# Kernel tuning notes

Measured on AMD Instinct MI355X. Metric: run time of the kernel, lower is better.

## Reference

```python
import jax, jax.numpy as jnp
import numpy as np
import hashlib

MAX_HASH_VALUE = 2 ** 8  # 256
BATCH, MAX_LEN, EMB, HID, VOCAB = 32, 512, 256, 1024, 32000


def _hash_mod(flat_ids, algo):
    # SHA digest interpreted little-endian; only value mod 256 matters for the
    # downstream (h1 + k*h2) % 256, and mod 256 of a little-endian int is just
    # the first digest byte. We keep the full int.from_bytes for faithfulness.
    return np.array(
        [int.from_bytes(algo(str(int(v)).encode()).digest(), 'little') % MAX_HASH_VALUE
         for v in flat_ids],
        dtype=np.int64,
    )


def setup_inputs() -> dict:
    key = jax.random.key(0)
    k1, k2, k3 = jax.random.split(key, 3)
    input_ids = jax.random.randint(k1, (BATCH, MAX_LEN), 0, VOCAB, dtype=jnp.int64)
    W = jax.random.normal(k2, (HID, EMB), dtype=jnp.float32) * (1.0 / np.sqrt(EMB))
    b = jax.random.normal(k3, (HID,), dtype=jnp.float32) * 0.01
    return {"input_ids": input_ids, "W": W, "b": b}


def reference(input_ids, W, b):
    ids = np.asarray(input_ids)            # [B, L] int
    B, L = ids.shape
    flat = ids.reshape(-1)
    h1 = _hash_mod(flat, hashlib.sha256).reshape(B, L)   # [B, L] in [0,256)
    h2 = _hash_mod(flat, hashlib.sha224).reshape(B, L)
    k = jnp.arange(EMB, dtype=jnp.int64)                 # [E]
    # hash3[b,l,k] = (h1 + k*h2) % 256
    hash3 = ((jnp.asarray(h1)[:, :, None] + k[None, None, :] * jnp.asarray(h2)[:, :, None])
             % MAX_HASH_VALUE).astype(jnp.float32)        # [B, L, E]
    out = jnp.einsum('ble,he->blh', hash3, W) + b        # [B, L, H]
    return out
```

## Files before the change

kernel.cpp:

```cpp
#include <hip/hip_runtime.h>
#include <stdint.h>

typedef short bf16x8 __attribute__((ext_vector_type(8)));
typedef float f32x16 __attribute__((ext_vector_type(16)));

#define EMB 256
#define HID 1024

#define ROTR(x,n) (((x)>>(n))|((x)<<(32-(n))))
#define S0F(x) (ROTR((x),7)^ROTR((x),18)^((x)>>3))
#define S1F(x) (ROTR((x),17)^ROTR((x),19)^((x)>>10))

#define RND1(Kc, Wt) do {                                                          \
    uint32_t t1_ = sh + (ROTR(se,6)^ROTR(se,11)^ROTR(se,25))                       \
                   + ((se&sf)^(~se&sg)) + (Kc) + (Wt);                             \
    uint32_t t2_ = (ROTR(sa,2)^ROTR(sa,13)^ROTR(sa,22))                            \
                   + ((sa&sb)^(sa&sc)^(sb&sc));                                    \
    sh=sg; sg=sf; sf=se; se=sd+t1_; sd=sc; sc=sb; sb=sa; sa=t1_+t2_; } while (0)

#define WSXS(a,b,c,d) ((a) += S0F(b) + (c) + S1F(d))

__device__ __forceinline__ uint32_t rbf(float x) {
    uint32_t b = __float_as_uint(x);
    return (b + 0x7FFFu + ((b >> 16) & 1u)) >> 16;
}
__device__ __forceinline__ uint4 pack8(float4 a, float4 b) {
    uint4 q;
    q.x = rbf(a.x) | (rbf(a.y) << 16);
    q.y = rbf(a.z) | (rbf(a.w) << 16);
    q.z = rbf(b.x) | (rbf(b.y) << 16);
    q.w = rbf(b.z) | (rbf(b.w) << 16);
    return q;
}

#define MFMA(av,bv,acc) __builtin_amdgcn_mfma_f32_32x32x16_bf16(av,bv,acc,0,0,0)

__global__ __launch_bounds__(256, 1) void fused_kernel(const uint32_t* __restrict__ ids32,
                                                       const float* __restrict__ W,
                                                       const float* __restrict__ bias,
                                                       float* __restrict__ out) {
    __shared__ uint4 Albuf[4096];
    __shared__ uint4 Blbuf[4096];
    uint32_t* redf = (uint32_t*)(Blbuf + 2048);

    const int bid = blockIdx.x;
    const int bm = bid >> 1;
    const int nb0 = (bid & 1) * 512;
    const int tid = (int)threadIdx.x;
    const int wv = tid >> 6, lane = tid & 63, lrow = lane & 31, lh = lane >> 5;
    const int wm = (wv >> 1) * 64, wn = (wv & 1) * 64;
    const int lga = (wv >> 1) * 2, lgb = (wv & 1) * 2;
    const int rr = tid >> 1;
    const uint32_t st = tid & 1;
    const int ag = rr >> 5, aslot = rr & 31;

    float4 stgA[16], stgB[16];

#define ISSUE(dst, cc) do {                                                        \
    const float4* ws_ = reinterpret_cast<const float4*>(                           \
        W + (size_t)(nb0 + ((cc) >> 1) * 128 + rr) * EMB + ((cc) & 1) * 128 + (int)st * 64); \
    _Pragma("unroll") for (int i_ = 0; i_ < 16; ++i_) dst[i_] = ws_[i_]; } while (0)

#define WRITEB(src, cc) do {                                                       \
    uint4* bb_ = Blbuf + ((cc) & 1) * 2048 + (ag * 8) * 64 + aslot;                \
    _Pragma("unroll") for (int q_ = 0; q_ < 4; ++q_) {                             \
        uint4 h0_ = pack8(src[q_ * 4 + 0], src[q_ * 4 + 1]);                       \
        uint4 h1_ = pack8(src[q_ * 4 + 2], src[q_ * 4 + 3]);                       \
        bb_[((int)st * 4 + q_) * 64]      = h0_;                                   \
        bb_[((int)st * 4 + q_) * 64 + 32] = h1_; } } while (0)

#define MFMA_CHUNK(cc) do {                                                        \
    const uint4* bb_ = Blbuf + ((cc) & 1) * 2048;                                  \
    _Pragma("unroll") for (int ks_ = 0; ks_ < 8; ++ks_) {                          \
        bf16x8 av0 = *reinterpret_cast<const bf16x8*>(&Albuf[(lga * 16 + ((cc) & 1) * 8 + ks_) * 64 + lane]); \
        bf16x8 av1 = *reinterpret_cast<const bf16x8*>(&Albuf[((lga + 1) * 16 + ((cc) & 1) * 8 + ks_) * 64 + lane]); \
        bf16x8 bv0 = *reinterpret_cast<const bf16x8*>(&bb_[(lgb * 8 + ks_) * 64 + lane]); \
        bf16x8 bv1 = *reinterpret_cast<const bf16x8*>(&bb_[((lgb + 1) * 8 + ks_) * 64 + lane]); \
        acc00 = MFMA(av0, bv0, acc00); acc01 = MFMA(av0, bv1, acc01);              \
        acc10 = MFMA(av1, bv0, acc10); acc11 = MFMA(av1, bv1, acc11); } } while (0)

#define STORE_SUB(ss, bj0_, bj1_) do {                                             \
    const int n0s_ = nb0 + (ss) * 128 + wn;                                        \
    _Pragma("unroll") for (int r_ = 0; r_ < 16; ++r_) {                            \
        const int rowl_ = (r_ & 3) + 8 * (r_ >> 2) + 4 * lh;                       \
        const size_t o0_ = (size_t)(bm * 128 + wm + rowl_) * HID;                  \
        const size_t o1_ = o0_ + 32 * HID;                                         \
        out[o0_ + n0s_ + lrow]      = acc00[r_] + bj0_;                            \
        out[o0_ + n0s_ + 32 + lrow] = acc01[r_] + bj1_;                            \
        out[o1_ + n0s_ + lrow]      = acc10[r_] + bj0_;                            \
        out[o1_ + n0s_ + 32 + lrow] = acc11[r_] + bj1_; }                          \
    acc00 = (f32x16)(0.0f); acc01 = (f32x16)(0.0f);                                \
    acc10 = (f32x16)(0.0f); acc11 = (f32x16)(0.0f); } while (0)

    ISSUE(stgA, 0);

    {
        const uint4* ids4 = reinterpret_cast<const uint4*>(ids32);
        uint4 da = ids4[tid], db = ids4[tid + 256];
        uint32_t z = da.y | da.w | db.y | db.w;
        unsigned long long m = __ballot(z != 0u);
        if (lane == 0) redf[wv] = (m != 0ull) ? 1u : 0u;
    }
    __syncthreads();
    const bool is64 = (redf[0] | redf[1] | redf[2] | redf[3]) == 0u;

    const int tok = bm * 128 + rr;
    const uint32_t v = is64 ? ids32[2 * tok] : ids32[tok];

    const uint32_t q4 = __umulhi(v, 0xD1B71759u) >> 13;
    const uint32_t r4 = v - q4 * 10000u;
    const uint32_t q3 = __umulhi(r4, 0x10624DD3u) >> 6;
    const uint32_t r3 = r4 - q3 * 1000u;
    const uint32_t q2 = __umulhi(r3, 0x51EB851Fu) >> 5;
    const uint32_t r2 = r3 - q2 * 100u;
    const uint32_t q1 = __umulhi(r2, 0xCCCCCCCDu) >> 3;
    const uint32_t q0 = r2 - q1 * 10u;
    const uint32_t nd = v >= 10000u ? 5u : v >= 1000u ? 4u : v >= 100u ? 3u
                         : v >= 10u ? 2u : 1u;
    uint64_t M = ((uint64_t)(q4 + '0') << 56) | ((uint64_t)(q3 + '0') << 48) |
                 ((uint64_t)(q2 + '0') << 40) | ((uint64_t)(q1 + '0') << 32) |
                 ((uint64_t)(q0 + '0') << 24) | ((uint64_t)0x80u << 16);
    M <<= 8u * (5u - nd);

    uint32_t w0 = (uint32_t)(M >> 32), w1 = (uint32_t)M;
    uint32_t w2 = 0, w3 = 0, w4 = 0, w5 = 0, w6 = 0, w7 = 0;
    uint32_t w8 = 0, w9 = 0, w10 = 0, w11 = 0, w12 = 0, w13 = 0, w14 = 0;
    uint32_t w15 = nd * 8u;

    uint32_t sa = st ? 0xc1059ed8u : 0x6a09e667u;
    uint32_t sb = st ? 0x367cd507u : 0xbb67ae85u;
    uint32_t sc = st ? 0x3070dd17u : 0x3c6ef372u;
    uint32_t sd = st ? 0xf70e5939u : 0xa54ff53au;
    uint32_t se = st ? 0xffc00b31u : 0x510e527fu;
    uint32_t sf = st ? 0x68581511u : 0x9b05688cu;
    uint32_t sg = st ? 0x64f98fa7u : 0x1f83d9abu;
    uint32_t sh = st ? 0xbefa4fa4u : 0x5be0cd19u;

    RND1(0x428a2f98u, w0);  RND1(0x71374491u, w1);  RND1(0xb5c0fbcfu, w2);
    RND1(0xe9b5dba5u, w3);  RND1(0x3956c25bu, w4);  RND1(0x59f111f1u, w5);
    RND1(0x923f82a4u, w6);  RND1(0xab1c5ed5u, w7);  RND1(0xd807aa98u, w8);
    RND1(0x12835b01u, w9);  RND1(0x243185beu, w10); RND1(0x550c7dc3u, w11);
    RND1(0x72be5d74u, w12); RND1(0x80deb1feu, w13); RND1(0x9bdc06a7u, w14);
    RND1(0xc19bf174u, w15);
    WSXS(w0,w1,w9,w14);    RND1(0xe49b69c1u, w0);
    WSXS(w1,w2,w10,w15);   RND1(0xefbe4786u, w1);
    WSXS(w2,w3,w11,w0);    RND1(0x0fc19dc6u, w2);
    WSXS(w3,w4,w12,w1);    RND1(0x240ca1ccu, w3);
    WSXS(w4,w5,w13,w2);    RND1(0x2de92c6fu, w4);
    WSXS(w5,w6,w14,w3);    RND1(0x4a7484aau, w5);
    WSXS(w6,w7,w15,w4);    RND1(0x5cb0a9dcu, w6);
    WSXS(w7,w8,w0,w5);     RND1(0x76f988dau, w7);
    WSXS(w8,w9,w1,w6);     RND1(0x983e5152u, w8);
    WSXS(w9,w10,w2,w7);    RND1(0xa831c66du, w9);
    WSXS(w10,w11,w3,w8);   RND1(0xb00327c8u, w10);
    WSXS(w11,w12,w4,w9);   RND1(0xbf597fc7u, w11);
    WSXS(w12,w13,w5,w10);  RND1(0xc6e00bf3u, w12);
    WSXS(w13,w14,w6,w11);  RND1(0xd5a79147u, w13);
    WSXS(w14,w15,w7,w12);  RND1(0x06ca6351u, w14);
    WSXS(w15,w0,w8,w13);   RND1(0x14292967u, w15);
    WSXS(w0,w1,w9,w14);    RND1(0x27b70a85u, w0);
    WSXS(w1,w2,w10,w15);   RND1(0x2e1b2138u, w1);
    WSXS(w2,w3,w11,w0);    RND1(0x4d2c6dfcu, w2);
    WSXS(w3,w4,w12,w1);    RND1(0x53380d13u, w3);
    WSXS(w4,w5,w13,w2);    RND1(0x650a7354u, w4);
    WSXS(w5,w6,w14,w3);    RND1(0x766a0abbu, w5);
    WSXS(w6,w7,w15,w4);    RND1(0x81c2c92eu, w6);
    WSXS(w7,w8,w0,w5);     RND1(0x92722c85u, w7);
    WSXS(w8,w9,w1,w6);     RND1(0xa2bfe8a1u, w8);
    WSXS(w9,w10,w2,w7);    RND1(0xa81a664bu, w9);
    WSXS(w10,w11,w3,w8);   RND1(0xc24b8b70u, w10);
    WSXS(w11,w12,w4,w9);   RND1(0xc76c51a3u, w11);
    WSXS(w12,w13,w5,w10);  RND1(0xd192e819u, w12);
    WSXS(w13,w14,w6,w11);  RND1(0xd6990624u, w13);
    WSXS(w14,w15,w7,w12);  RND1(0xf40e3585u, w14);
    WSXS(w15,w0,w8,w13);   RND1(0x106aa070u, w15);
    WSXS(w0,w1,w9,w14);    RND1(0x19a4c116u, w0);
    WSXS(w1,w2,w10,w15);   RND1(0x1e376c08u, w1);
    WSXS(w2,w3,w11,w0);    RND1(0x2748774cu, w2);
    WSXS(w3,w4,w12,w1);    RND1(0x34b0bcb5u, w3);
    WSXS(w4,w5,w13,w2);    RND1(0x391c0cb3u, w4);
    WSXS(w5,w6,w14,w3);    RND1(0x4ed8aa4au, w5);
    WSXS(w6,w7,w15,w4);    RND1(0x5b9cca4fu, w6);
    WSXS(w7,w8,w0,w5);     RND1(0x682e6ff3u, w7);
    WSXS(w8,w9,w1,w6);     RND1(0x748f82eeu, w8);
    WSXS(w9,w10,w2,w7);    RND1(0x78a5636fu, w9);
    WSXS(w10,w11,w3,w8);   RND1(0x84c87814u, w10);
    WSXS(w11,w12,w4,w9);   RND1(0x8cc70208u, w11);
    WSXS(w12,w13,w5,w10);  RND1(0x90befffau, w12);
    WSXS(w13,w14,w6,w11);  RND1(0xa4506cebu, w13);
    WSXS(w14,w15,w7,w12);  RND1(0xbef9a3f7u, w14);
    WSXS(w15,w0,w8,w13);   RND1(0xc67178f2u, w15);

    const uint32_t hv = ((st ? 0xc1059ed8u : 0x6a09e667u) + sa) >> 24;
    const uint32_t hvo = __shfl_xor(hv, 1);
    const uint32_t hv1 = st ? hvo : hv;
    const uint32_t hv2 = st ? hv : hvo;

    {
        uint32_t val = (hv1 + (st ? ((hv2 << 7) & 255u) : 0u)) & 255u;
        const int kfb = (int)st * 8;
#define PAIR(dst) { uint32_t lo_ = val; uint32_t hi_ = (val + hv2) & 255u;        \
                    val = (hi_ + hv2) & 255u;                                     \
                    dst = (__float_as_uint((float)lo_) >> 16) |                   \
                          (__float_as_uint((float)hi_) & 0xFFFF0000u); }
#pragma unroll
        for (int q = 0; q < 8; ++q) {
            uint32_t c0_, c1_, c2_, c3_, c4_, c5_, c6_, c7_;
            PAIR(c0_); PAIR(c1_); PAIR(c2_); PAIR(c3_);
            PAIR(c4_); PAIR(c5_); PAIR(c6_); PAIR(c7_);
            uint4 qa; qa.x = c0_; qa.y = c1_; qa.z = c2_; qa.w = c3_;
            uint4 qb; qb.x = c4_; qb.y = c5_; qb.z = c6_; qb.w = c7_;
            Albuf[(ag * 16 + kfb + q) * 64 + aslot]      = qa;
            Albuf[(ag * 16 + kfb + q) * 64 + aslot + 32] = qb;
        }
#undef PAIR
    }

    WRITEB(stgA, 0);
    ISSUE(stgB, 1);

    const float b00 = bias[nb0 +   0 + wn + lrow], b01 = bias[nb0 +   0 + wn + 32 + lrow];
    const float b10 = bias[nb0 + 128 + wn + lrow], b11 = bias[nb0 + 128 + wn + 32 + lrow];
    const float b20 = bias[nb0 + 256 + wn + lrow], b21 = bias[nb0 + 256 + wn + 32 + lrow];
    const float b30 = bias[nb0 + 384 + wn + lrow], b31 = bias[nb0 + 384 + wn + 32 + lrow];

    f32x16 acc00 = (f32x16)(0.0f), acc01 = (f32x16)(0.0f);
    f32x16 acc10 = (f32x16)(0.0f), acc11 = (f32x16)(0.0f);

    __syncthreads();

    ISSUE(stgA, 2);  MFMA_CHUNK(0);                         WRITEB(stgB, 1); __syncthreads();
    ISSUE(stgB, 3);  MFMA_CHUNK(1); STORE_SUB(0, b00, b01); WRITEB(stgA, 2); __syncthreads();
    ISSUE(stgA, 4);  MFMA_CHUNK(2);                         WRITEB(stgB, 3); __syncthreads();
    ISSUE(stgB, 5);  MFMA_CHUNK(3); STORE_SUB(1, b10, b11); WRITEB(stgA, 4); __syncthreads();
    ISSUE(stgA, 6);  MFMA_CHUNK(4);                         WRITEB(stgB, 5); __syncthreads();
    ISSUE(stgB, 7);  MFMA_CHUNK(5); STORE_SUB(2, b20, b21); WRITEB(stgA, 6); __syncthreads();
                     MFMA_CHUNK(6);                         WRITEB(stgB, 7); __syncthreads();
                     MFMA_CHUNK(7); STORE_SUB(3, b30, b31);

#undef ISSUE
#undef WRITEB
#undef MFMA_CHUNK
#undef STORE_SUB
}

extern "C" void kernel_launch(void* const* d_in, const int* in_sizes, int n_in,
                              void* d_out, int out_size, void* d_ws, size_t ws_size,
                              hipStream_t stream) {
    const uint32_t* ids32 = (const uint32_t*)d_in[0];
    const float* W = (const float*)d_in[1];
    const float* bias = (const float*)d_in[2];
    float* out = (float*)d_out;
    (void)d_ws; (void)ws_size; (void)in_sizes; (void)n_in; (void)out_size;

    fused_kernel<<<256, 256, 0, stream>>>(ids32, W, bias, out);
}
```

Measured before the change: 36.40 us.

## Remap W staging to wave-contiguous LDS writes and use LDS-only barriers

Reassigns which thread loads which W elements so each wave writes a contiguous, lane-indexed LDS region with a single pack8 store per step, instead of the two-slot interleaved scatter. It also replaces __syncthreads with a barrier that waits only on LDS counters (lgkmcnt), so in-flight global W prefetches and output stores no longer have to drain at each barrier. The risk is correctness of the new mapping against the MFMA B-fragment layout, and the weaker barrier relies on global data being consumed only after later waits.

```diff
diff --git a/kernel.cpp b/kernel.cpp
--- a/kernel.cpp
+++ b/kernel.cpp
@@ -34,6 +34,11 @@
 }
 
 #define MFMA(av,bv,acc) __builtin_amdgcn_mfma_f32_32x32x16_bf16(av,bv,acc,0,0,0)
+
+#define BARRIER_LGKM() do {                                                        \
+    asm volatile("s_waitcnt lgkmcnt(0)" ::: "memory");                             \
+    __builtin_amdgcn_s_barrier();                                                  \
+    __builtin_amdgcn_sched_barrier(0); } while (0)
 
 __global__ __launch_bounds__(256, 1) void fused_kernel(const uint32_t* __restrict__ ids32,
                                                        const float* __restrict__ W,
@@ -57,17 +62,17 @@
     float4 stgA[16], stgB[16];
 
 #define ISSUE(dst, cc) do {                                                        \
-    const float4* ws_ = reinterpret_cast<const float4*>(                           \
-        W + (size_t)(nb0 + ((cc) >> 1) * 128 + rr) * EMB + ((cc) & 1) * 128 + (int)st * 64); \
-    _Pragma("unroll") for (int i_ = 0; i_ < 16; ++i_) dst[i_] = ws_[i_]; } while (0)
+    const float4* ws_ = reinterpret_cast<const float4*>(W)                         \
+        + ((size_t)(nb0 + ((cc) >> 1) * 128 + wv * 32 + lrow) * 64)                \
+        + ((cc) & 1) * 32 + lh * 2;                                                \
+    _Pragma("unroll") for (int q_ = 0; q_ < 8; ++q_) {                             \
+        dst[2 * q_]     = ws_[q_ * 4];                                             \
+        dst[2 * q_ + 1] = ws_[q_ * 4 + 1]; } } while (0)
 
 #define WRITEB(src, cc) do {                                                       \
-    uint4* bb_ = Blbuf + ((cc) & 1) * 2048 + (ag * 8) * 64 + aslot;                \
-    _Pragma("unroll") for (int q_ = 0; q_ < 4; ++q_) {                             \
-        uint4 h0_ = pack8(src[q_ * 4 + 0], src[q_ * 4 + 1]);                       \
-        uint4 h1_ = pack8(src[q_ * 4 + 2], src[q_ * 4 + 3]);                       \
-        bb_[((int)st * 4 + q_) * 64]      = h0_;                                   \
-        bb_[((int)st * 4 + q_) * 64 + 32] = h1_; } } while (0)
+    uint4* bb_ = Blbuf + ((cc) & 1) * 2048 + wv * 512 + lane;                      \
+    _Pragma("unroll") for (int q_ = 0; q_ < 8; ++q_)                               \
+        bb_[q_ * 64] = pack8(src[2 * q_], src[2 * q_ + 1]); } while (0)
 
 #define MFMA_CHUNK(cc) do {                                                        \
     const uint4* bb_ = Blbuf + ((cc) & 1) * 2048;                                  \
@@ -101,7 +106,7 @@
         unsigned long long m = __ballot(z != 0u);
         if (lane == 0) redf[wv] = (m != 0ull) ? 1u : 0u;
     }
-    __syncthreads();
+    BARRIER_LGKM();
     const bool is64 = (redf[0] | redf[1] | redf[2] | redf[3]) == 0u;
 
     const int tok = bm * 128 + rr;
@@ -227,15 +232,15 @@
     f32x16 acc00 = (f32x16)(0.0f), acc01 = (f32x16)(0.0f);
     f32x16 acc10 = (f32x16)(0.0f), acc11 = (f32x16)(0.0f);
 
-    __syncthreads();
-
-    ISSUE(stgA, 2);  MFMA_CHUNK(0);                         WRITEB(stgB, 1); __syncthreads();
-    ISSUE(stgB, 3);  MFMA_CHUNK(1); STORE_SUB(0, b00, b01); WRITEB(stgA, 2); __syncthreads();
-    ISSUE(stgA, 4);  MFMA_CHUNK(2);                         WRITEB(stgB, 3); __syncthreads();
-    ISSUE(stgB, 5);  MFMA_CHUNK(3); STORE_SUB(1, b10, b11); WRITEB(stgA, 4); __syncthreads();
-    ISSUE(stgA, 6);  MFMA_CHUNK(4);                         WRITEB(stgB, 5); __syncthreads();
-    ISSUE(stgB, 7);  MFMA_CHUNK(5); STORE_SUB(2, b20, b21); WRITEB(stgA, 6); __syncthreads();
-                     MFMA_CHUNK(6);                         WRITEB(stgB, 7); __syncthreads();
+    BARRIER_LGKM();
+
+    ISSUE(stgA, 2);  MFMA_CHUNK(0);                         WRITEB(stgB, 1); BARRIER_LGKM();
+    ISSUE(stgB, 3);  MFMA_CHUNK(1); STORE_SUB(0, b00, b01); WRITEB(stgA, 2); BARRIER_LGKM();
+    ISSUE(stgA, 4);  MFMA_CHUNK(2);                         WRITEB(stgB, 3); BARRIER_LGKM();
+    ISSUE(stgB, 5);  MFMA_CHUNK(3); STORE_SUB(1, b10, b11); WRITEB(stgA, 4); BARRIER_LGKM();
+    ISSUE(stgA, 6);  MFMA_CHUNK(4);                         WRITEB(stgB, 5); BARRIER_LGKM();
+    ISSUE(stgB, 7);  MFMA_CHUNK(5); STORE_SUB(2, b20, b21); WRITEB(stgA, 6); BARRIER_LGKM();
+                     MFMA_CHUNK(6);                         WRITEB(stgB, 7); BARRIER_LGKM();
                      MFMA_CHUNK(7); STORE_SUB(3, b30, b31);
 
 #undef ISSUE
```

Measured after the change: 39.36 us. 8.1% more time.

## Halve M tile to 64 rows and run two blocks per CU

Applied to the files above, without the earlier changes.

Shrinks each block's output tile from 128 to 64 rows, doubling the grid to 512 blocks. Each wave now computes a 32x64 sub-tile with two accumulators instead of four. Shared buffers are halved and launch bounds are raised to two blocks per CU, so more waves can hide memory latency. W is staged in 64-wide K chunks over 16 pipeline steps, and only half the threads run the SHA hashing. The cost is that every W tile is re-read by twice as many blocks, with more barriers per block.

```diff
diff --git a/kernel.cpp b/kernel.cpp
--- a/kernel.cpp
+++ b/kernel.cpp
@@ -35,62 +35,54 @@
 
 #define MFMA(av,bv,acc) __builtin_amdgcn_mfma_f32_32x32x16_bf16(av,bv,acc,0,0,0)
 
-__global__ __launch_bounds__(256, 1) void fused_kernel(const uint32_t* __restrict__ ids32,
+__global__ __launch_bounds__(256, 2) void fused_kernel(const uint32_t* __restrict__ ids32,
                                                        const float* __restrict__ W,
                                                        const float* __restrict__ bias,
                                                        float* __restrict__ out) {
-    __shared__ uint4 Albuf[4096];
-    __shared__ uint4 Blbuf[4096];
-    uint32_t* redf = (uint32_t*)(Blbuf + 2048);
+    __shared__ uint4 Albuf[2048];
+    __shared__ uint4 Blbuf[2048];
+    uint32_t* redf = (uint32_t*)(Blbuf + 1024);
 
     const int bid = blockIdx.x;
     const int bm = bid >> 1;
     const int nb0 = (bid & 1) * 512;
     const int tid = (int)threadIdx.x;
     const int wv = tid >> 6, lane = tid & 63, lrow = lane & 31, lh = lane >> 5;
-    const int wm = (wv >> 1) * 64, wn = (wv & 1) * 64;
-    const int lga = (wv >> 1) * 2, lgb = (wv & 1) * 2;
-    const int rr = tid >> 1;
-    const uint32_t st = tid & 1;
-    const int ag = rr >> 5, aslot = rr & 31;
-
-    float4 stgA[16], stgB[16];
+    const int lgb = (wv & 1) * 2;
+    const int mrow0 = bm * 64 + (wv >> 1) * 32;
+
+    float4 stgA[8], stgB[8];
 
 #define ISSUE(dst, cc) do {                                                        \
-    const float4* ws_ = reinterpret_cast<const float4*>(                           \
-        W + (size_t)(nb0 + ((cc) >> 1) * 128 + rr) * EMB + ((cc) & 1) * 128 + (int)st * 64); \
-    _Pragma("unroll") for (int i_ = 0; i_ < 16; ++i_) dst[i_] = ws_[i_]; } while (0)
+    const float4* ws_ = reinterpret_cast<const float4*>(W)                         \
+        + ((size_t)(nb0 + ((cc) >> 2) * 128 + wv * 32 + lrow) * 64)                \
+        + ((cc) & 3) * 16 + lh * 2;                                                \
+    _Pragma("unroll") for (int w_ = 0; w_ < 4; ++w_) {                             \
+        dst[2 * w_]     = ws_[w_ * 4];                                             \
+        dst[2 * w_ + 1] = ws_[w_ * 4 + 1]; } } while (0)
 
 #define WRITEB(src, cc) do {                                                       \
-    uint4* bb_ = Blbuf + ((cc) & 1) * 2048 + (ag * 8) * 64 + aslot;                \
-    _Pragma("unroll") for (int q_ = 0; q_ < 4; ++q_) {                             \
-        uint4 h0_ = pack8(src[q_ * 4 + 0], src[q_ * 4 + 1]);                       \
-        uint4 h1_ = pack8(src[q_ * 4 + 2], src[q_ * 4 + 3]);                       \
-        bb_[((int)st * 4 + q_) * 64]      = h0_;                                   \
-        bb_[((int)st * 4 + q_) * 64 + 32] = h1_; } } while (0)
+    uint4* bb_ = Blbuf + ((cc) & 1) * 1024 + wv * 256 + lane;                      \
+    _Pragma("unroll") for (int w_ = 0; w_ < 4; ++w_)                               \
+        bb_[w_ * 64] = pack8(src[2 * w_], src[2 * w_ + 1]); } while (0)
 
 #define MFMA_CHUNK(cc) do {                                                        \
-    const uint4* bb_ = Blbuf + ((cc) & 1) * 2048;                                  \
-    _Pragma("unroll") for (int ks_ = 0; ks_ < 8; ++ks_) {                          \
-        bf16x8 av0 = *reinterpret_cast<const bf16x8*>(&Albuf[(lga * 16 + ((cc) & 1) * 8 + ks_) * 64 + lane]); \
-        bf16x8 av1 = *reinterpret_cast<const bf16x8*>(&Albuf[((lga + 1) * 16 + ((cc) & 1) * 8 + ks_) * 64 + lane]); \
-        bf16x8 bv0 = *reinterpret_cast<const bf16x8*>(&bb_[(lgb * 8 + ks_) * 64 + lane]); \
-        bf16x8 bv1 = *reinterpret_cast<const bf16x8*>(&bb_[((lgb + 1) * 8 + ks_) * 64 + lane]); \
-        acc00 = MFMA(av0, bv0, acc00); acc01 = MFMA(av0, bv1, acc01);              \
-        acc10 = MFMA(av1, bv0, acc10); acc11 = MFMA(av1, bv1, acc11); } } while (0)
+    const uint4* bb_ = Blbuf + ((cc) & 1) * 1024;                                  \
+    const uint4* aa_ = Albuf + ((size_t)((wv >> 1) * 16 + ((cc) & 3) * 4)) * 64 + lane; \
+    _Pragma("unroll") for (int kf_ = 0; kf_ < 4; ++kf_) {                          \
+        bf16x8 av  = *reinterpret_cast<const bf16x8*>(&aa_[kf_ * 64]);             \
+        bf16x8 bv0 = *reinterpret_cast<const bf16x8*>(&bb_[(lgb * 4 + kf_) * 64 + lane]); \
+        bf16x8 bv1 = *reinterpret_cast<const bf16x8*>(&bb_[((lgb + 1) * 4 + kf_) * 64 + lane]); \
+        acc0 = MFMA(av, bv0, acc0); acc1 = MFMA(av, bv1, acc1); } } while (0)
 
 #define STORE_SUB(ss, bj0_, bj1_) do {                                             \
-    const int n0s_ = nb0 + (ss) * 128 + wn;                                        \
+    const int col_ = nb0 + (ss) * 128 + lgb * 32 + lrow;                           \
     _Pragma("unroll") for (int r_ = 0; r_ < 16; ++r_) {                            \
         const int rowl_ = (r_ & 3) + 8 * (r_ >> 2) + 4 * lh;                       \
-        const size_t o0_ = (size_t)(bm * 128 + wm + rowl_) * HID;                  \
-        const size_t o1_ = o0_ + 32 * HID;                                         \
-        out[o0_ + n0s_ + lrow]      = acc00[r_] + bj0_;                            \
-        out[o0_ + n0s_ + 32 + lrow] = acc01[r_] + bj1_;                            \
-        out[o1_ + n0s_ + lrow]      = acc10[r_] + bj0_;                            \
-        out[o1_ + n0s_ + 32 + lrow] = acc11[r_] + bj1_; }                          \
-    acc00 = (f32x16)(0.0f); acc01 = (f32x16)(0.0f);                                \
-    acc10 = (f32x16)(0.0f); acc11 = (f32x16)(0.0f); } while (0)
+        const size_t o_ = (size_t)(mrow0 + rowl_) * HID + col_;                    \
+        out[o_]      = acc0[r_] + bj0_;                                            \
+        out[o_ + 32] = acc1[r_] + bj1_; }                                          \
+    acc0 = (f32x16)(0.0f); acc1 = (f32x16)(0.0f); } while (0)
 
     ISSUE(stgA, 0);
 
@@ -104,99 +96,108 @@
     __syncthreads();
     const bool is64 = (redf[0] | redf[1] | redf[2] | redf[3]) == 0u;
 
-    const int tok = bm * 128 + rr;
-    const uint32_t v = is64 ? ids32[2 * tok] : ids32[tok];
-
-    const uint32_t q4 = __umulhi(v, 0xD1B71759u) >> 13;
-    const uint32_t r4 = v - q4 * 10000u;
-    const uint32_t q3 = __umulhi(r4, 0x10624DD3u) >> 6;
-    const uint32_t r3 = r4 - q3 * 1000u;
-    const uint32_t q2 = __umulhi(r3, 0x51EB851Fu) >> 5;
-    const uint32_t r2 = r3 - q2 * 100u;
-    const uint32_t q1 = __umulhi(r2, 0xCCCCCCCDu) >> 3;
-    const uint32_t q0 = r2 - q1 * 10u;
-    const uint32_t nd = v >= 10000u ? 5u : v >= 1000u ? 4u : v >= 100u ? 3u
-                         : v >= 10u ? 2u : 1u;
-    uint64_t M = ((uint64_t)(q4 + '0') << 56) | ((uint64_t)(q3 + '0') << 48) |
-                 ((uint64_t)(q2 + '0') << 40) | ((uint64_t)(q1 + '0') << 32) |
-                 ((uint64_t)(q0 + '0') << 24) | ((uint64_t)0x80u << 16);
-    M <<= 8u * (5u - nd);
-
-    uint32_t w0 = (uint32_t)(M >> 32), w1 = (uint32_t)M;
-    uint32_t w2 = 0, w3 = 0, w4 = 0, w5 = 0, w6 = 0, w7 = 0;
-    uint32_t w8 = 0, w9 = 0, w10 = 0, w11 = 0, w12 = 0, w13 = 0, w14 = 0;
-    uint32_t w15 = nd * 8u;
-
-    uint32_t sa = st ? 0xc1059ed8u : 0x6a09e667u;
-    uint32_t sb = st ? 0x367cd507u : 0xbb67ae85u;
-    uint32_t sc = st ? 0x3070dd17u : 0x3c6ef372u;
-    uint32_t sd = st ? 0xf70e5939u : 0xa54ff53au;
-    uint32_t se = st ? 0xffc00b31u : 0x510e527fu;
-    uint32_t sf = st ? 0x68581511u : 0x9b05688cu;
-    uint32_t sg = st ? 0x64f98fa7u : 0x1f83d9abu;
-    uint32_t sh = st ? 0xbefa4fa4u : 0x5be0cd19u;
-
-    RND1(0x428a2f98u, w0);  RND1(0x71374491u, w1);  RND1(0xb5c0fbcfu, w2);
-    RND1(0xe9b5dba5u, w3);  RND1(0x3956c25bu, w4);  RND1(0x59f111f1u, w5);
-    RND1(0x923f82a4u, w6);  RND1(0xab1c5ed5u, w7);  RND1(0xd807aa98u, w8);
-    RND1(0x12835b01u, w9);  RND1(0x243185beu, w10); RND1(0x550c7dc3u, w11);
-    RND1(0x72be5d74u, w12); RND1(0x80deb1feu, w13); RND1(0x9bdc06a7u, w14);
-    RND1(0xc19bf174u, w15);
-    WSXS(w0,w1,w9,w14);    RND1(0xe49b69c1u, w0);
-    WSXS(w1,w2,w10,w15);   RND1(0xefbe4786u, w1);
-    WSXS(w2,w3,w11,w0);    RND1(0x0fc19dc6u, w2);
-    WSXS(w3,w4,w12,w1);    RND1(0x240ca1ccu, w3);
-    WSXS(w4,w5,w13,w2);    RND1(0x2de92c6fu, w4);
-    WSXS(w5,w6,w14,w3);    RND1(0x4a7484aau, w5);
-    WSXS(w6,w7,w15,w4);    RND1(0x5cb0a9dcu, w6);
-    WSXS(w7,w8,w0,w5);     RND1(0x76f988dau, w7);
-    WSXS(w8,w9,w1,w6);     RND1(0x983e5152u, w8);
-    WSXS(w9,w10,w2,w7);    RND1(0xa831c66du, w9);
-    WSXS(w10,w11,w3,w8);   RND1(0xb00327c8u, w10);
-    WSXS(w11,w12,w4,w9);   RND1(0xbf597fc7u, w11);
-    WSXS(w12,w13,w5,w10);  RND1(0xc6e00bf3u, w12);
-    WSXS(w13,w14,w6,w11);  RND1(0xd5a79147u, w13);
-    WSXS(w14,w15,w7,w12);  RND1(0x06ca6351u, w14);
-    WSXS(w15,w0,w8,w13);   RND1(0x14292967u, w15);
-    WSXS(w0,w1,w9,w14);    RND1(0x27b70a85u, w0);
-    WSXS(w1,w2,w10,w15);   RND1(0x2e1b2138u, w1);
-    WSXS(w2,w3,w11,w0);    RND1(0x4d2c6dfcu, w2);
-    WSXS(w3,w4,w12,w1);    RND1(0x53380d13u, w3);
-    WSXS(w4,w5,w13,w2);    RND1(0x650a7354u, w4);
-    WSXS(w5,w6,w14,w3);    RND1(0x766a0abbu, w5);
-    WSXS(w6,w7,w15,w4);    RND1(0x81c2c92eu, w6);
-    WSXS(w7,w8,w0,w5);     RND1(0x92722c85u, w7);
-    WSXS(w8,w9,w1,w6);     RND1(0xa2bfe8a1u, w8);
-    WSXS(w9,w10,w2,w7);    RND1(0xa81a664bu, w9);
-    WSXS(w10,w11,w3,w8);   RND1(0xc24b8b70u, w10);
-    WSXS(w11,w12,w4,w9);   RND1(0xc76c51a3u, w11);
-    WSXS(w12,w13,w5,w10);  RND1(0xd192e819u, w12);
-    WSXS(w13,w14,w6,w11);  RND1(0xd6990624u, w13);
-    WSXS(w14,w15,w7,w12);  RND1(0xf40e3585u, w14);
-    WSXS(w15,w0,w8,w13);   RND1(0x106aa070u, w15);
-    WSXS(w0,w1,w9,w14);    RND1(0x19a4c116u, w0);
-    WSXS(w1,w2,w10,w15);   RND1(0x1e376c08u, w1);
-    WSXS(w2,w3,w11,w0);    RND1(0x2748774cu, w2);
-    WSXS(w3,w4,w12,w1);    RND1(0x34b0bcb5u, w3);
-    WSXS(w4,w5,w13,w2);    RND1(0x391c0cb3u, w4);
-    WSXS(w5,w6,w14,w3);    RND1(0x4ed8aa4au, w5);
-    WSXS(w6,w7,w15,w4);    RND1(0x5b9cca4fu, w6);
-    WSXS(w7,w8,w0,w5);     RND1(0x682e6ff3u, w7);
-    WSXS(w8,w9,w1,w6);     RND1(0x748f82eeu, w8);
-    WSXS(w9,w10,w2,w7);    RND1(0x78a5636fu, w9);
-    WSXS(w10,w11,w3,w8);   RND1(0x84c87814u, w10);
-    WSXS(w11,w12,w4,w9);   RND1(0x8cc70208u, w11);
-    WSXS(w12,w13,w5,w10);  RND1(0x90befffau, w12);
-    WSXS(w13,w14,w6,w11);  RND1(0xa4506cebu, w13);
-    WSXS(w14,w15,w7,w12);  RND1(0xbef9a3f7u, w14);
-    WSXS(w15,w0,w8,w13);   RND1(0xc67178f2u, w15);
-
-    const uint32_t hv = ((st ? 0xc1059ed8u : 0x6a09e667u) + sa) >> 24;
-    const uint32_t hvo = __shfl_xor(hv, 1);
-    const uint32_t hv1 = st ? hvo : hv;
-    const uint32_t hv2 = st ? hv : hvo;
-
-    {
+    const int cbase = nb0 + lgb * 32 + lrow;
+    const float bb00 = bias[cbase +   0], bb01 = bias[cbase +  32];
+    const float bb10 = bias[cbase + 128], bb11 = bias[cbase + 160];
+    const float bb20 = bias[cbase + 256], bb21 = bias[cbase + 288];
+    const float bb30 = bias[cbase + 384], bb31 = bias[cbase + 416];
+
+    if (tid < 128) {
+        const int rr = tid >> 1;
+        const uint32_t st = tid & 1;
+        const int tok = bm * 64 + rr;
+        const uint32_t v = is64 ? ids32[2 * tok] : ids32[tok];
+
+        const uint32_t q4 = __umulhi(v, 0xD1B71759u) >> 13;
+        const uint32_t r4 = v - q4 * 10000u;
+        const uint32_t q3 = __umulhi(r4, 0x10624DD3u) >> 6;
+        const uint32_t r3 = r4 - q3 * 1000u;
+        const uint32_t q2 = __umulhi(r3, 0x51EB851Fu) >> 5;
+        const uint32_t r2 = r3 - q2 * 100u;
+        const uint32_t q1 = __umulhi(r2, 0xCCCCCCCDu) >> 3;
+        const uint32_t q0 = r2 - q1 * 10u;
+        const uint32_t nd = v >= 10000u ? 5u : v >= 1000u ? 4u : v >= 100u ? 3u
+                             : v >= 10u ? 2u : 1u;
+        uint64_t M = ((uint64_t)(q4 + '0') << 56) | ((uint64_t)(q3 + '0') << 48) |
+                     ((uint64_t)(q2 + '0') << 40) | ((uint64_t)(q1 + '0') << 32) |
+                     ((uint64_t)(q0 + '0') << 24) | ((uint64_t)0x80u << 16);
+        M <<= 8u * (5u - nd);
+
+        uint32_t w0 = (uint32_t)(M >> 32), w1 = (uint32_t)M;
+        uint32_t w2 = 0, w3 = 0, w4 = 0, w5 = 0, w6 = 0, w7 = 0;
+        uint32_t w8 = 0, w9 = 0, w10 = 0, w11 = 0, w12 = 0, w13 = 0, w14 = 0;
+        uint32_t w15 = nd * 8u;
+
+        uint32_t sa = st ? 0xc1059ed8u : 0x6a09e667u;
+        uint32_t sb = st ? 0x367cd507u : 0xbb67ae85u;
+        uint32_t sc = st ? 0x3070dd17u : 0x3c6ef372u;
+        uint32_t sd = st ? 0xf70e5939u : 0xa54ff53au;
+        uint32_t se = st ? 0xffc00b31u : 0x510e527fu;
+        uint32_t sf = st ? 0x68581511u : 0x9b05688cu;
+        uint32_t sg = st ? 0x64f98fa7u : 0x1f83d9abu;
+        uint32_t sh = st ? 0xbefa4fa4u : 0x5be0cd19u;
+
+        RND1(0x428a2f98u, w0);  RND1(0x71374491u, w1);  RND1(0xb5c0fbcfu, w2);
+        RND1(0xe9b5dba5u, w3);  RND1(0x3956c25bu, w4);  RND1(0x59f111f1u, w5);
+        RND1(0x923f82a4u, w6);  RND1(0xab1c5ed5u, w7);  RND1(0xd807aa98u, w8);
+        RND1(0x12835b01u, w9);  RND1(0x243185beu, w10); RND1(0x550c7dc3u, w11);
+        RND1(0x72be5d74u, w12); RND1(0x80deb1feu, w13); RND1(0x9bdc06a7u, w14);
+        RND1(0xc19bf174u, w15);
+        WSXS(w0,w1,w9,w14);    RND1(0xe49b69c1u, w0);
+        WSXS(w1,w2,w10,w15);   RND1(0xefbe4786u, w1);
+        WSXS(w2,w3,w11,w0);    RND1(0x0fc19dc6u, w2);
+        WSXS(w3,w4,w12,w1);    RND1(0x240ca1ccu, w3);
+        WSXS(w4,w5,w13,w2);    RND1(0x2de92c6fu, w4);
+        WSXS(w5,w6,w14,w3);    RND1(0x4a7484aau, w5);
+        WSXS(w6,w7,w15,w4);    RND1(0x5cb0a9dcu, w6);
+        WSXS(w7,w8,w0,w5);     RND1(0x76f988dau, w7);
+        WSXS(w8,w9,w1,w6);     RND1(0x983e5152u, w8);
+        WSXS(w9,w10,w2,w7);    RND1(0xa831c66du, w9);
+        WSXS(w10,w11,w3,w8);   RND1(0xb00327c8u, w10);
+        WSXS(w11,w12,w4,w9);   RND1(0xbf597fc7u, w11);
+        WSXS(w12,w13,w5,w10);  RND1(0xc6e00bf3u, w12);
+        WSXS(w13,w14,w6,w11);  RND1(0xd5a79147u, w13);
+        WSXS(w14,w15,w7,w12);  RND1(0x06ca6351u, w14);
+        WSXS(w15,w0,w8,w13);   RND1(0x14292967u, w15);
+        WSXS(w0,w1,w9,w14);    RND1(0x27b70a85u, w0);
+        WSXS(w1,w2,w10,w15);   RND1(0x2e1b2138u, w1);
+        WSXS(w2,w3,w11,w0);    RND1(0x4d2c6dfcu, w2);
+        WSXS(w3,w4,w12,w1);    RND1(0x53380d13u, w3);
+        WSXS(w4,w5,w13,w2);    RND1(0x650a7354u, w4);
+        WSXS(w5,w6,w14,w3);    RND1(0x766a0abbu, w5);
+        WSXS(w6,w7,w15,w4);    RND1(0x81c2c92eu, w6);
+        WSXS(w7,w8,w0,w5);     RND1(0x92722c85u, w7);
+        WSXS(w8,w9,w1,w6);     RND1(0xa2bfe8a1u, w8);
+        WSXS(w9,w10,w2,w7);    RND1(0xa81a664bu, w9);
+        WSXS(w10,w11,w3,w8);   RND1(0xc24b8b70u, w10);
+        WSXS(w11,w12,w4,w9);   RND1(0xc76c51a3u, w11);
+        WSXS(w12,w13,w5,w10);  RND1(0xd192e819u, w12);
+        WSXS(w13,w14,w6,w11);  RND1(0xd6990624u, w13);
+        WSXS(w14,w15,w7,w12);  RND1(0xf40e3585u, w14);
+        WSXS(w15,w0,w8,w13);   RND1(0x106aa070u, w15);
+        WSXS(w0,w1,w9,w14);    RND1(0x19a4c116u, w0);
+        WSXS(w1,w2,w10,w15);   RND1(0x1e376c08u, w1);
+        WSXS(w2,w3,w11,w0);    RND1(0x2748774cu, w2);
+        WSXS(w3,w4,w12,w1);    RND1(0x34b0bcb5u, w3);
+        WSXS(w4,w5,w13,w2);    RND1(0x391c0cb3u, w4);
+        WSXS(w5,w6,w14,w3);    RND1(0x4ed8aa4au, w5);
+        WSXS(w6,w7,w15,w4);    RND1(0x5b9cca4fu, w6);
+        WSXS(w7,w8,w0,w5);     RND1(0x682e6ff3u, w7);
+        WSXS(w8,w9,w1,w6);     RND1(0x748f82eeu, w8);
+        WSXS(w9,w10,w2,w7);    RND1(0x78a5636fu, w9);
+        WSXS(w10,w11,w3,w8);   RND1(0x84c87814u, w10);
+        WSXS(w11,w12,w4,w9);   RND1(0x8cc70208u, w11);
+        WSXS(w12,w13,w5,w10);  RND1(0x90befffau, w12);
+        WSXS(w13,w14,w6,w11);  RND1(0xa4506cebu, w13);
+        WSXS(w14,w15,w7,w12);  RND1(0xbef9a3f7u, w14);
+        WSXS(w15,w0,w8,w13);   RND1(0xc67178f2u, w15);
+
+        const uint32_t hv = ((st ? 0xc1059ed8u : 0x6a09e667u) + sa) >> 24;
+        const uint32_t hvo = __shfl_xor(hv, 1);
+        const uint32_t hv1 = st ? hvo : hv;
+        const uint32_t hv2 = st ? hv : hvo;
+
+        const int ag = rr >> 5, aslot = rr & 31;
         uint32_t val = (hv1 + (st ? ((hv2 << 7) & 255u) : 0u)) & 255u;
         const int kfb = (int)st * 8;
 #define PAIR(dst) { uint32_t lo_ = val; uint32_t hi_ = (val + hv2) & 255u;        \
@@ -219,24 +220,26 @@
     WRITEB(stgA, 0);
     ISSUE(stgB, 1);
 
-    const float b00 = bias[nb0 +   0 + wn + lrow], b01 = bias[nb0 +   0 + wn + 32 + lrow];
-    const float b10 = bias[nb0 + 128 + wn + lrow], b11 = bias[nb0 + 128 + wn + 32 + lrow];
-    const float b20 = bias[nb0 + 256 + wn + lrow], b21 = bias[nb0 + 256 + wn + 32 + lrow];
-    const float b30 = bias[nb0 + 384 + wn + lrow], b31 = bias[nb0 + 384 + wn + 32 + lrow];
-
-    f32x16 acc00 = (f32x16)(0.0f), acc01 = (f32x16)(0.0f);
-    f32x16 acc10 = (f32x16)(0.0f), acc11 = (f32x16)(0.0f);
+    f32x16 acc0 = (f32x16)(0.0f), acc1 = (f32x16)(0.0f);
 
     __syncthreads();
 
-    ISSUE(stgA, 2);  MFMA_CHUNK(0);                         WRITEB(stgB, 1); __syncthreads();
-    ISSUE(stgB, 3);  MFMA_CHUNK(1); STORE_SUB(0, b00, b01); WRITEB(stgA, 2); __syncthreads();
-    ISSUE(stgA, 4);  MFMA_CHUNK(2);                         WRITEB(stgB, 3); __syncthreads();
-    ISSUE(stgB, 5);  MFMA_CHUNK(3); STORE_SUB(1, b10, b11); WRITEB(stgA, 4); __syncthreads();
-    ISSUE(stgA, 6);  MFMA_CHUNK(4);                         WRITEB(stgB, 5); __syncthreads();
-    ISSUE(stgB, 7);  MFMA_CHUNK(5); STORE_SUB(2, b20, b21); WRITEB(stgA, 6); __syncthreads();
-                     MFMA_CHUNK(6);                         WRITEB(stgB, 7); __syncthreads();
-                     MFMA_CHUNK(7); STORE_SUB(3, b30, b31);
+    ISSUE(stgA,  2); MFMA_CHUNK(0);                           WRITEB(stgB,  1); __syncthreads();
+    ISSUE(stgB,  3); MFMA_CHUNK(1);                           WRITEB(stgA,  2); __syncthreads();
+    ISSUE(stgA,  4); MFMA_CHUNK(2);                           WRITEB(stgB,  3); __syncthreads();
+    ISSUE(stgB,  5); MFMA_CHUNK(3);  STORE_SUB(0, bb00, bb01); WRITEB(stgA,  4); __syncthreads();
+    ISSUE(stgA,  6); MFMA_CHUNK(4);                           WRITEB(stgB,  5); __syncthreads();
+    ISSUE(stgB,  7); MFMA_CHUNK(5);                           WRITEB(stgA,  6); __syncthreads();
+    ISSUE(stgA,  8); MFMA_CHUNK(6);                           WRITEB(stgB,  7); __syncthreads();
+    ISSUE(stgB,  9); MFMA_CHUNK(7);  STORE_SUB(1, bb10, bb11); WRITEB(stgA,  8); __syncthreads();
+    ISSUE(stgA, 10); MFMA_CHUNK(8);                           WRITEB(stgB,  9); __syncthreads();
+    ISSUE(stgB, 11); MFMA_CHUNK(9);                           WRITEB(stgA, 10); __syncthreads();
+    ISSUE(stgA, 12); MFMA_CHUNK(10);                          WRITEB(stgB, 11); __syncthreads();
+    ISSUE(stgB, 13); MFMA_CHUNK(11); STORE_SUB(2, bb20, bb21); WRITEB(stgA, 12); __syncthreads();
+    ISSUE(stgA, 14); MFMA_CHUNK(12);                          WRITEB(stgB, 13); __syncthreads();
+    ISSUE(stgB, 15); MFMA_CHUNK(13);                          WRITEB(stgA, 14); __syncthreads();
+                     MFMA_CHUNK(14);                          WRITEB(stgB, 15); __syncthreads();
+                     MFMA_CHUNK(15); STORE_SUB(3, bb30, bb31);
 
 #undef ISSUE
 #undef WRITEB
@@ -253,5 +256,5 @@
     float* out = (float*)d_out;
     (void)d_ws; (void)ws_size; (void)in_sizes; (void)n_in; (void)out_size;
 
-    fused_kernel<<<256, 256, 0, stream>>>(ids32, W, bias, out);
-}
+    fused_kernel<<<512, 256, 0, stream>>>(ids32, W, bias, out);
+}
```

Measured after the change: 46.27 us. +27.1%, slower.

## Pre-convert W to bf16 MFMA layout in separate kernel, stream B from global

Applied to the files above, without the earlier changes.

Adds a prep kernel that converts W to bf16 once per call and writes it to workspace in the MFMA fragment layout. The main kernel then reads B fragments straight from global/L2 instead of staging through LDS with per-block conversion. The grid doubles to 512 blocks with 2 blocks per CU, and output stores become nontemporal. This removes the redundant per-block W conversion and the LDS double buffering, at the cost of an extra launch and relying on L2 for B reuse.

```diff
diff --git a/kernel.cpp b/kernel.cpp
--- a/kernel.cpp
+++ b/kernel.cpp
@@ -3,9 +3,13 @@
 
 typedef short bf16x8 __attribute__((ext_vector_type(8)));
 typedef float f32x16 __attribute__((ext_vector_type(16)));
+typedef unsigned short ushort_t;
 
 #define EMB 256
 #define HID 1024
+#define NTOK 16384
+
+#define WS_W_OFF 0
 
 #define ROTR(x,n) (((x)>>(n))|((x)<<(32-(n))))
 #define S0F(x) (ROTR((x),7)^ROTR((x),18)^((x)>>3))
@@ -35,64 +39,33 @@
 
 #define MFMA(av,bv,acc) __builtin_amdgcn_mfma_f32_32x32x16_bf16(av,bv,acc,0,0,0)
 
-__global__ __launch_bounds__(256, 1) void fused_kernel(const uint32_t* __restrict__ ids32,
-                                                       const float* __restrict__ W,
+__global__ __launch_bounds__(256) void prep_kernel(const float* __restrict__ W,
+                                                   ushort_t* __restrict__ Wf) {
+    const int t = blockIdx.x * 256 + threadIdx.x;
+    const int h = t >> 4;
+    const int kk = t & 15;
+    const float4* wsrc = reinterpret_cast<const float4*>(W + h * EMB + kk * 16);
+    float4 a = wsrc[0], b = wsrc[1], c = wsrc[2], d = wsrc[3];
+    uint4 qa = pack8(a, b);
+    uint4 qb = pack8(c, d);
+    uint4* wbase = reinterpret_cast<uint4*>(Wf) + ((size_t)(h >> 5) * 16 + kk) * 64 + (h & 31);
+    wbase[0]  = qa;
+    wbase[32] = qb;
+}
+
+__global__ __launch_bounds__(256, 2) void fused_kernel(const uint32_t* __restrict__ ids32,
+                                                       const ushort_t* __restrict__ Wf,
                                                        const float* __restrict__ bias,
                                                        float* __restrict__ out) {
     __shared__ uint4 Albuf[4096];
-    __shared__ uint4 Blbuf[4096];
-    uint32_t* redf = (uint32_t*)(Blbuf + 2048);
+    __shared__ uint32_t redf[4];
 
     const int bid = blockIdx.x;
-    const int bm = bid >> 1;
-    const int nb0 = (bid & 1) * 512;
+    const int bm = bid >> 2;
+    const int nb0 = (bid & 3) * 256;
     const int tid = (int)threadIdx.x;
     const int wv = tid >> 6, lane = tid & 63, lrow = lane & 31, lh = lane >> 5;
-    const int wm = (wv >> 1) * 64, wn = (wv & 1) * 64;
-    const int lga = (wv >> 1) * 2, lgb = (wv & 1) * 2;
-    const int rr = tid >> 1;
-    const uint32_t st = tid & 1;
-    const int ag = rr >> 5, aslot = rr & 31;
-
-    float4 stgA[16], stgB[16];
-
-#define ISSUE(dst, cc) do {                                                        \
-    const float4* ws_ = reinterpret_cast<const float4*>(                           \
-        W + (size_t)(nb0 + ((cc) >> 1) * 128 + rr) * EMB + ((cc) & 1) * 128 + (int)st * 64); \
-    _Pragma("unroll") for (int i_ = 0; i_ < 16; ++i_) dst[i_] = ws_[i_]; } while (0)
-
-#define WRITEB(src, cc) do {                                                       \
-    uint4* bb_ = Blbuf + ((cc) & 1) * 2048 + (ag * 8) * 64 + aslot;                \
-    _Pragma("unroll") for (int q_ = 0; q_ < 4; ++q_) {                             \
-        uint4 h0_ = pack8(src[q_ * 4 + 0], src[q_ * 4 + 1]);                       \
-        uint4 h1_ = pack8(src[q_ * 4 + 2], src[q_ * 4 + 3]);                       \
-        bb_[((int)st * 4 + q_) * 64]      = h0_;                                   \
-        bb_[((int)st * 4 + q_) * 64 + 32] = h1_; } } while (0)
-
-#define MFMA_CHUNK(cc) do {                                                        \
-    const uint4* bb_ = Blbuf + ((cc) & 1) * 2048;                                  \
-    _Pragma("unroll") for (int ks_ = 0; ks_ < 8; ++ks_) {                          \
-        bf16x8 av0 = *reinterpret_cast<const bf16x8*>(&Albuf[(lga * 16 + ((cc) & 1) * 8 + ks_) * 64 + lane]); \
-        bf16x8 av1 = *reinterpret_cast<const bf16x8*>(&Albuf[((lga + 1) * 16 + ((cc) & 1) * 8 + ks_) * 64 + lane]); \
-        bf16x8 bv0 = *reinterpret_cast<const bf16x8*>(&bb_[(lgb * 8 + ks_) * 64 + lane]); \
-        bf16x8 bv1 = *reinterpret_cast<const bf16x8*>(&bb_[((lgb + 1) * 8 + ks_) * 64 + lane]); \
-        acc00 = MFMA(av0, bv0, acc00); acc01 = MFMA(av0, bv1, acc01);              \
-        acc10 = MFMA(av1, bv0, acc10); acc11 = MFMA(av1, bv1, acc11); } } while (0)
-
-#define STORE_SUB(ss, bj0_, bj1_) do {                                             \
-    const int n0s_ = nb0 + (ss) * 128 + wn;                                        \
-    _Pragma("unroll") for (int r_ = 0; r_ < 16; ++r_) {                            \
-        const int rowl_ = (r_ & 3) + 8 * (r_ >> 2) + 4 * lh;                       \
-        const size_t o0_ = (size_t)(bm * 128 + wm + rowl_) * HID;                  \
-        const size_t o1_ = o0_ + 32 * HID;                                         \
-        out[o0_ + n0s_ + lrow]      = acc00[r_] + bj0_;                            \
-        out[o0_ + n0s_ + 32 + lrow] = acc01[r_] + bj1_;                            \
-        out[o1_ + n0s_ + lrow]      = acc10[r_] + bj0_;                            \
-        out[o1_ + n0s_ + 32 + lrow] = acc11[r_] + bj1_; }                          \
-    acc00 = (f32x16)(0.0f); acc01 = (f32x16)(0.0f);                                \
-    acc10 = (f32x16)(0.0f); acc11 = (f32x16)(0.0f); } while (0)
-
-    ISSUE(stgA, 0);
+    const int wm = wv >> 1, wn = wv & 1;
 
     {
         const uint4* ids4 = reinterpret_cast<const uint4*>(ids32);
@@ -104,6 +77,8 @@
     __syncthreads();
     const bool is64 = (redf[0] | redf[1] | redf[2] | redf[3]) == 0u;
 
+    const int rr = tid >> 1;
+    const uint32_t st = tid & 1;
     const int tok = bm * 128 + rr;
     const uint32_t v = is64 ? ids32[2 * tok] : ids32[tok];
 
@@ -197,6 +172,7 @@
     const uint32_t hv2 = st ? hv : hvo;
 
     {
+        const int ag = rr >> 5, aslot = rr & 31;
         uint32_t val = (hv1 + (st ? ((hv2 << 7) & 255u) : 0u)) & 255u;
         const int kfb = (int)st * 8;
 #define PAIR(dst) { uint32_t lo_ = val; uint32_t hi_ = (val + hv2) & 255u;        \
@@ -216,32 +192,46 @@
 #undef PAIR
     }
 
-    WRITEB(stgA, 0);
-    ISSUE(stgB, 1);
-
-    const float b00 = bias[nb0 +   0 + wn + lrow], b01 = bias[nb0 +   0 + wn + 32 + lrow];
-    const float b10 = bias[nb0 + 128 + wn + lrow], b11 = bias[nb0 + 128 + wn + 32 + lrow];
-    const float b20 = bias[nb0 + 256 + wn + lrow], b21 = bias[nb0 + 256 + wn + 32 + lrow];
-    const float b30 = bias[nb0 + 384 + wn + lrow], b31 = bias[nb0 + 384 + wn + 32 + lrow];
-
-    f32x16 acc00 = (f32x16)(0.0f), acc01 = (f32x16)(0.0f);
-    f32x16 acc10 = (f32x16)(0.0f), acc11 = (f32x16)(0.0f);
+    const int cb = nb0 + wn * 64 + lrow;
+    const float bs00 = bias[cb],       bs01 = bias[cb + 32];
+    const float bs10 = bias[cb + 128], bs11 = bias[cb + 160];
 
     __syncthreads();
 
-    ISSUE(stgA, 2);  MFMA_CHUNK(0);                         WRITEB(stgB, 1); __syncthreads();
-    ISSUE(stgB, 3);  MFMA_CHUNK(1); STORE_SUB(0, b00, b01); WRITEB(stgA, 2); __syncthreads();
-    ISSUE(stgA, 4);  MFMA_CHUNK(2);                         WRITEB(stgB, 3); __syncthreads();
-    ISSUE(stgB, 5);  MFMA_CHUNK(3); STORE_SUB(1, b10, b11); WRITEB(stgA, 4); __syncthreads();
-    ISSUE(stgA, 6);  MFMA_CHUNK(4);                         WRITEB(stgB, 5); __syncthreads();
-    ISSUE(stgB, 7);  MFMA_CHUNK(5); STORE_SUB(2, b20, b21); WRITEB(stgA, 6); __syncthreads();
-                     MFMA_CHUNK(6);                         WRITEB(stgB, 7); __syncthreads();
-                     MFMA_CHUNK(7); STORE_SUB(3, b30, b31);
-
-#undef ISSUE
-#undef WRITEB
-#undef MFMA_CHUNK
-#undef STORE_SUB
+    const bf16x8* bfr = reinterpret_cast<const bf16x8*>(Wf);
+    const bf16x8* alr = reinterpret_cast<const bf16x8*>(Albuf);
+    const int agA0 = (wm * 2) * 16, agA1 = (wm * 2 + 1) * 16;
+    const int m0 = bm * 128 + wm * 64;
+
+#define DO_SUB(sub, bj0_, bj1_) do {                                               \
+    const int gb0_ = (nb0 >> 5) + (sub) * 4 + wn * 2;                              \
+    f32x16 a00 = (f32x16)(0.0f), a01 = (f32x16)(0.0f);                             \
+    f32x16 a10 = (f32x16)(0.0f), a11 = (f32x16)(0.0f);                             \
+    _Pragma("unroll 2")                                                            \
+    for (int kf = 0; kf < 16; ++kf) {                                              \
+        bf16x8 bv0 = bfr[((size_t)(gb0_ * 16 + kf)) * 64 + lane];                  \
+        bf16x8 bv1 = bfr[((size_t)((gb0_ + 1) * 16 + kf)) * 64 + lane];            \
+        bf16x8 av0 = alr[(agA0 + kf) * 64 + lane];                                 \
+        bf16x8 av1 = alr[(agA1 + kf) * 64 + lane];                                 \
+        a00 = MFMA(av0, bv0, a00); a01 = MFMA(av0, bv1, a01);                      \
+        a10 = MFMA(av1, bv0, a10); a11 = MFMA(av1, bv1, a11);                      \
+    }                                                                              \
+    const int col_ = nb0 + (sub) * 128 + wn * 64 + lrow;                           \
+    _Pragma("unroll")                                                              \
+    for (int r_ = 0; r_ < 16; ++r_) {                                              \
+        const int rowl_ = (r_ & 3) + 8 * (r_ >> 2) + 4 * lh;                       \
+        const size_t o0_ = (size_t)(m0 + rowl_) * HID + col_;                      \
+        const size_t o1_ = o0_ + (size_t)32 * HID;                                 \
+        __builtin_nontemporal_store(a00[r_] + bj0_, &out[o0_]);                    \
+        __builtin_nontemporal_store(a01[r_] + bj1_, &out[o0_ + 32]);               \
+        __builtin_nontemporal_store(a10[r_] + bj0_, &out[o1_]);                    \
+        __builtin_nontemporal_store(a11[r_] + bj1_, &out[o1_ + 32]);               \
+    } } while (0)
+
+    DO_SUB(0, bs00, bs01);
+    DO_SUB(1, bs10, bs11);
+
+#undef DO_SUB
 }
 
 extern "C" void kernel_launch(void* const* d_in, const int* in_sizes, int n_in,
@@ -251,7 +241,9 @@
     const float* W = (const float*)d_in[1];
     const float* bias = (const float*)d_in[2];
     float* out = (float*)d_out;
-    (void)d_ws; (void)ws_size; (void)in_sizes; (void)n_in; (void)out_size;
-
-    fused_kernel<<<256, 256, 0, stream>>>(ids32, W, bias, out);
-}
+    ushort_t* Wf = (ushort_t*)((char*)d_ws + WS_W_OFF);
+    (void)in_sizes; (void)n_in; (void)out_size; (void)ws_size;
+
+    prep_kernel<<<64, 256, 0, stream>>>(W, Wf);
+    fused_kernel<<<512, 256, 0, stream>>>(ids32, Wf, bias, out);
+}
```

Result: faster. 34.98 us (-3.9%).
